# Kernel optimization log

Hardware: AMD Instinct MI355X
Metric: run time of the kernel (lower is better)

## Reference

```python
import jax, jax.numpy as jnp
import numpy as np

DIM = 512
NUM_HEADS = 16
HEAD_DIM = DIM // NUM_HEADS
RES = (32, 32)
SEQ_SCALE = float(np.log(RES[0] * RES[1]))  # seq_length_scale buffer
TABLE = (2 * RES[0] - 1) * (2 * RES[1] - 1)  # 3969
EPS = 1e-12


def setup_inputs() -> dict:
    key = jax.random.key(0)
    ks = jax.random.split(key, 12)
    B, N, C = 8, RES[0] * RES[1], DIM
    s = 0.02
    return {
        "x": jax.random.normal(ks[0], (B, N, C), dtype=jnp.float32),
        "_h": RES[0],
        "_w": RES[1],
        "relative_pos_index": jax.random.randint(ks[1], (N, N), 0, TABLE, dtype=jnp.int32),
        "relative_coords_table": jax.random.uniform(ks[2], (TABLE, 2), dtype=jnp.float32, minval=-1.0, maxval=1.0),
        "qkv_w": jax.random.normal(ks[3], (3 * C, C), dtype=jnp.float32) * s,
        "qkv_b": jnp.zeros((3 * C,), dtype=jnp.float32),
        "proj_w": jax.random.normal(ks[4], (C, C), dtype=jnp.float32) * s,
        "proj_b": jnp.zeros((C,), dtype=jnp.float32),
        "temperature": jnp.full((NUM_HEADS, 1, 1), float(np.log(np.expm1(1.0 / 0.24))), dtype=jnp.float32),
        "query_embedding": jax.random.normal(ks[5], (NUM_HEADS, 1, HEAD_DIM), dtype=jnp.float32) * s,
        "cpb_fc1_w": jax.random.normal(ks[6], (512, 2), dtype=jnp.float32) * s,
        "cpb_fc1_b": jnp.zeros((512,), dtype=jnp.float32),
        "cpb_fc2_w": jax.random.normal(ks[7], (NUM_HEADS, 512), dtype=jnp.float32) * s,
        "cpb_fc2_b": jnp.zeros((NUM_HEADS,), dtype=jnp.float32),
    }


def _l2norm(t):
    # F.normalize(t, dim=-1): x / max(||x||, eps)
    n = jnp.sqrt(jnp.sum(t * t, axis=-1, keepdims=True))
    return t / jnp.maximum(n, EPS)


def reference(x, _h, _w, relative_pos_index, relative_coords_table,
              qkv_w, qkv_b, proj_w, proj_b, temperature, query_embedding,
              cpb_fc1_w, cpb_fc1_b, cpb_fc2_w, cpb_fc2_b):
    B, N, C = x.shape
    H, hd = NUM_HEADS, HEAD_DIM
    # qkv projection -> [B, N, 3H, hd] -> [B, 3H, N, hd]
    qkv = (x @ qkv_w.T + qkv_b).reshape(B, N, 3 * H, hd).transpose(0, 2, 1, 3)
    q, k, v = jnp.split(qkv, 3, axis=1)  # each [B, H, N, hd]
    # CPB MLP relative bias: [T,2] -> [T,H] -> gather -> [H,N,N]
    t = jax.nn.relu(relative_coords_table @ cpb_fc1_w.T + cpb_fc1_b) @ cpb_fc2_w.T + cpb_fc2_b
    rel_bias = t[relative_pos_index].transpose(2, 0, 1)  # [H, N, N]
    # cosine attention with learned softplus temperature and query embedding
    scale = jax.nn.softplus(temperature) * SEQ_SCALE  # [H,1,1]
    qn = (_l2norm(q) + query_embedding[None]) * scale[None]
    kn = _l2norm(k)
    attn = jnp.einsum('bhnd,bhmd->bhnm', qn, kn) + rel_bias[None]
    attn = jax.nn.softmax(attn, axis=-1)
    out = jnp.einsum('bhnm,bhmd->bhnd', attn, v)  # [B,H,N,hd]
    out = out.transpose(0, 2, 1, 3).reshape(B, N, C)
    return out @ proj_w.T + proj_b
```

## Files before the change

kernel.cpp:

```cpp
#include <hip/hip_runtime.h>
#include <cstdint>
#include <cstddef>

typedef _Float16 f16;
typedef _Float16 f16x4 __attribute__((ext_vector_type(4)));
typedef _Float16 f16x8 __attribute__((ext_vector_type(8)));
typedef float f32x4 __attribute__((ext_vector_type(4)));

#define MFMA32(a,b,c) __builtin_amdgcn_mfma_f32_16x16x32_f16((a),(b),(c),0,0,0)
#define MFMA16(a,b,c) __builtin_amdgcn_mfma_f32_16x16x16f16((a),(b),(c),0,0,0)

__device__ __forceinline__ void gload_lds16(const f16* g, f16* l) {
  __builtin_amdgcn_global_load_lds(
      (const __attribute__((address_space(1))) unsigned int*)g,
      (__attribute__((address_space(3))) unsigned int*)l, 16, 0, 0);
}

static constexpr size_t OFF_TCPB = 0;
static constexpr size_t OFF_BIAS = 262144;
static constexpr size_t OFF_XHI  = OFF_BIAS + 33554432;
static constexpr size_t OFF_XLO  = OFF_XHI + 8388608;
static constexpr size_t OFF_WHI  = OFF_XLO + 8388608;
static constexpr size_t OFF_WLO  = OFF_WHI + 1572864;
static constexpr size_t OFF_PW   = OFF_WLO + 1572864;
static constexpr size_t OFF_QHI  = OFF_PW  + 524288;
static constexpr size_t OFF_QLO  = OFF_QHI + 8388608;
static constexpr size_t OFF_KHI  = OFF_QLO + 8388608;
static constexpr size_t OFF_KLO  = OFF_KHI + 8388608;
static constexpr size_t OFF_VT   = OFF_KLO + 8388608;
static constexpr size_t OFF_AO   = OFF_VT  + 8388608;

__global__ __launch_bounds__(256) void k_convert(
    const float* __restrict__ x, const float* __restrict__ qw, const float* __restrict__ pwf,
    f16* __restrict__ xhi, f16* __restrict__ xlo,
    f16* __restrict__ whi, f16* __restrict__ wlo, f16* __restrict__ pw)
{
  int i = blockIdx.x * 256 + threadIdx.x;
  const float4* src; f16* dh; f16* dl; int j;
  if (i < 1048576)      { j = i;           src = (const float4*)x;   dh = xhi; dl = xlo; }
  else if (i < 1245184) { j = i - 1048576; src = (const float4*)qw;  dh = whi; dl = wlo; }
  else                  { j = i - 1245184; src = (const float4*)pwf; dh = pw;  dl = nullptr; }
  float4 v = src[j];
  f16x4 h;
  h[0] = (f16)v.x; h[1] = (f16)v.y; h[2] = (f16)v.z; h[3] = (f16)v.w;
  ((f16x4*)dh)[j] = h;
  if (dl) {
    f16x4 l;
    l[0] = (f16)(v.x - (float)h[0]); l[1] = (f16)(v.y - (float)h[1]);
    l[2] = (f16)(v.z - (float)h[2]); l[3] = (f16)(v.w - (float)h[3]);
    ((f16x4*)dl)[j] = l;
  }
}

__global__ __launch_bounds__(256) void k_cpb(
    const float* __restrict__ table, const float* __restrict__ w1, const float* __restrict__ b1,
    const float* __restrict__ w2, const float* __restrict__ b2, float* __restrict__ t_out)
{
  const int r = blockIdx.x * 4 + (threadIdx.x >> 6);
  const int lane = threadIdx.x & 63;
  if (r >= 3969) return;
  const float c0 = table[2*r], c1 = table[2*r+1];
  const int j0 = lane * 8;
  float h[8];
#pragma unroll
  for (int jj = 0; jj < 8; jj++) {
    int j = j0 + jj;
    float v = c0 * w1[2*j] + c1 * w1[2*j+1] + b1[j];
    h[jj] = v > 0.0f ? v : 0.0f;
  }
  float acc[16];
#pragma unroll
  for (int o = 0; o < 16; o++) {
    const float4* wp = (const float4*)(w2 + o*512 + j0);
    float4 a = wp[0], bb = wp[1];
    acc[o] = a.x*h[0] + a.y*h[1] + a.z*h[2] + a.w*h[3]
           + bb.x*h[4] + bb.y*h[5] + bb.z*h[6] + bb.w*h[7];
  }
#pragma unroll
  for (int o = 0; o < 16; o++) {
    float v = acc[o];
    for (int s = 1; s < 64; s <<= 1) v += __shfl_xor(v, s, 64);
    acc[o] = v;
  }
  if (lane == 0) {
#pragma unroll
    for (int o = 0; o < 16; o++) t_out[r*16 + o] = acc[o] + b2[o];
  }
}

__global__ __launch_bounds__(256) void k_bias(
    const int* __restrict__ idx, const float* __restrict__ t_cpb, f16* __restrict__ bias_t)
{
  const int m4 = blockIdx.x >> 6, ng = blockIdx.x & 63;
  const int h = threadIdx.x >> 4, nl = threadIdx.x & 15;
  const int n = ng*16 + nl;
  int4 I = *(const int4*)(idx + (size_t)n*1024 + m4*4);
  f16x4 o;
  o[0] = (f16)t_cpb[I.x*16 + h];
  o[1] = (f16)t_cpb[I.y*16 + h];
  o[2] = (f16)t_cpb[I.z*16 + h];
  o[3] = (f16)t_cpb[I.w*16 + h];
  *(f16x4*)(bias_t + (((size_t)h*256 + m4)*1024 + n)*4) = o;
}

__global__ __launch_bounds__(256) void k_qkv(
    const f16* __restrict__ xhi, const f16* __restrict__ xlo,
    const f16* __restrict__ whi, const f16* __restrict__ wlo,
    const float* __restrict__ qkvb, const float* __restrict__ temp, const float* __restrict__ qe,
    f16* __restrict__ qh_o, f16* __restrict__ ql_o,
    f16* __restrict__ kh_o, f16* __restrict__ vt_o)
{
  __shared__ __align__(16) f16 Ah[8][64][8];
  __shared__ __align__(16) f16 Al[8][64][8];
  __shared__ __align__(16) f16 Bh[8][64][8];
  __shared__ __align__(16) f16 Bl[8][64][8];
  const int tid = threadIdx.x, lane = tid & 63, w = tid >> 6;
  const int rsel = lane & 15, ksel = lane >> 4;
  const int bx = blockIdx.x & 63, by = blockIdx.x >> 6;
  const int m0 = bx << 7, n0 = by << 7;
  const bool SPLIT = (by < 8);

  const size_t aoff = (size_t)(m0 + w*32 + rsel)*512 + ksel*8;
  const size_t boff = (size_t)(n0 + w*32 + rsel)*512 + ksel*8;
  const f16 *gA0 = xhi + aoff,  *gA1 = gA0 + 16*512;
  const f16 *gAl0 = xlo + aoff, *gAl1 = gAl0 + 16*512;
  const f16 *gB0 = whi + boff,  *gB1 = gB0 + 16*512;
  const f16 *gBl0 = wlo + boff, *gBl1 = gBl0 + 16*512;
  f16 *lA0 = &Ah[2*w][0][0],  *lA1 = &Ah[2*w+1][0][0];
  f16 *lAl0 = &Al[2*w][0][0], *lAl1 = &Al[2*w+1][0][0];
  f16 *lB0 = &Bh[2*w][0][0],  *lB1 = &Bh[2*w+1][0][0];
  f16 *lBl0 = &Bl[2*w][0][0], *lBl1 = &Bl[2*w+1][0][0];

  const f32x4 zero = {0.f, 0.f, 0.f, 0.f};
  f32x4 acc[4][4];
#pragma unroll
  for (int mt = 0; mt < 4; mt++)
#pragma unroll
    for (int nt = 0; nt < 4; nt++) acc[mt][nt] = zero;

  const int mb4 = (w & 1) * 4, nb4 = (w >> 1) * 4;
  for (int k0 = 0; k0 < 512; k0 += 32) {
    __syncthreads();
    gload_lds16(gA0 + k0, lA0);
    gload_lds16(gA1 + k0, lA1);
    gload_lds16(gB0 + k0, lB0);
    gload_lds16(gB1 + k0, lB1);
    if (SPLIT) {
      gload_lds16(gAl0 + k0, lAl0);
      gload_lds16(gAl1 + k0, lAl1);
      gload_lds16(gBl0 + k0, lBl0);
      gload_lds16(gBl1 + k0, lBl1);
    }
    __syncthreads();
    f16x8 bhf[4], blf[4];
#pragma unroll
    for (int nt = 0; nt < 4; nt++) bhf[nt] = ((const f16x8*)&Bh[nb4+nt][0][0])[lane];
    if (SPLIT) {
#pragma unroll
      for (int nt = 0; nt < 4; nt++) blf[nt] = ((const f16x8*)&Bl[nb4+nt][0][0])[lane];
#pragma unroll
      for (int mt = 0; mt < 4; mt++) {
        f16x8 ah = ((const f16x8*)&Ah[mb4+mt][0][0])[lane];
        f16x8 al = ((const f16x8*)&Al[mb4+mt][0][0])[lane];
#pragma unroll
        for (int nt = 0; nt < 4; nt++) {
          acc[mt][nt] = MFMA32(al, bhf[nt], acc[mt][nt]);
          acc[mt][nt] = MFMA32(ah, blf[nt], acc[mt][nt]);
          acc[mt][nt] = MFMA32(ah, bhf[nt], acc[mt][nt]);
        }
      }
    } else {
#pragma unroll
      for (int mt = 0; mt < 4; mt++) {
        f16x8 ah = ((const f16x8*)&Ah[mb4+mt][0][0])[lane];
#pragma unroll
        for (int nt = 0; nt < 4; nt++)
          acc[mt][nt] = MFMA32(ah, bhf[nt], acc[mt][nt]);
      }
    }
  }

  const int mbase = m0 + (w & 1)*64, nbase = n0 + (w >> 1)*64;
  float bc[4];
#pragma unroll
  for (int nt = 0; nt < 4; nt++) bc[nt] = qkvb[nbase + nt*16 + rsel];
#pragma unroll
  for (int mt = 0; mt < 4; mt++)
#pragma unroll
    for (int nt = 0; nt < 4; nt++)
#pragma unroll
      for (int r = 0; r < 4; r++) acc[mt][nt][r] += bc[nt];

  if (by < 8) {
    const bool ISQ = (by < 4);
#pragma unroll
    for (int pair = 0; pair < 2; pair++) {
      const int h = ((nbase - (ISQ ? 0 : 512)) >> 5) + pair;
      float sc = 0.f, qe0 = 0.f, qe1 = 0.f;
      if (ISQ) {
        sc  = log1pf(__expf(temp[h])) * 6.93147180559945f;
        qe0 = qe[h*32 + rsel];
        qe1 = qe[h*32 + 16 + rsel];
      }
      f16* dh = ISQ ? qh_o : kh_o;
#pragma unroll
      for (int mt = 0; mt < 4; mt++) {
        float ss[4];
#pragma unroll
        for (int r = 0; r < 4; r++) {
          float a = acc[mt][2*pair][r], b = acc[mt][2*pair+1][r];
          ss[r] = a*a + b*b;
        }
        for (int s = 1; s < 16; s <<= 1) {
#pragma unroll
          for (int r = 0; r < 4; r++) ss[r] += __shfl_xor(ss[r], s, 64);
        }
#pragma unroll
        for (int r = 0; r < 4; r++) {
          float rn = 1.0f / fmaxf(sqrtf(ss[r]), 1e-12f);
          int m = mbase + mt*16 + ksel*4 + r;
          int b_ = m >> 10, p = m & 1023;
          size_t base = ((size_t)(b_*16 + h)*1024 + p)*32;
          float v0 = acc[mt][2*pair][r] * rn;
          float v1 = acc[mt][2*pair+1][r] * rn;
          if (ISQ) { v0 = (v0 + qe0) * sc; v1 = (v1 + qe1) * sc; }
          f16 h0 = (f16)v0, h1 = (f16)v1;
          dh[base + rsel]      = h0;
          dh[base + 16 + rsel] = h1;
          if (ISQ) {
            ql_o[base + rsel]      = (f16)(v0 - (float)h0);
            ql_o[base + 16 + rsel] = (f16)(v1 - (float)h1);
          }
        }
      }
    }
  } else {
#pragma unroll
    for (int mt = 0; mt < 4; mt++) {
      int m = mbase + mt*16 + ksel*4;
      int b_ = m >> 10, p = m & 1023;
#pragma unroll
      for (int nt = 0; nt < 4; nt++) {
        int n = nbase + nt*16 + rsel;
        int g = (n - 1024) >> 5, d = n & 31;
        f16x4 pk;
#pragma unroll
        for (int r = 0; r < 4; r++) pk[r] = (f16)acc[mt][nt][r];
        *(f16x4*)(vt_o + ((size_t)(b_*16 + g)*32 + d)*1024 + p) = pk;
      }
    }
  }
}

__global__ __launch_bounds__(256, 4) void k_attn(
    const f16* __restrict__ qhi, const f16* __restrict__ qlo,
    const f16* __restrict__ khi, const f16* __restrict__ vt,
    const f16* __restrict__ bias_t,
    f16* __restrict__ po0, f16* __restrict__ po1,
    float2* __restrict__ ml0, float2* __restrict__ ml1)
{
  __shared__ __align__(16) f16 OT[4][32][40];
  const int lane = threadIdx.x & 63, w = threadIdx.x >> 6;
  const int rsel = lane & 15, ksel = lane >> 4;
  const int bid = blockIdx.x;
  const int qt = bid & 7, split = (bid >> 3) & 1, bh = bid >> 4;
  const int h = bh & 15;
  const int q0 = qt*128 + w*32;
  const int mstart = split * 512;

  f16x8 Qh[2], Ql[2];
#pragma unroll
  for (int c = 0; c < 2; c++) {
    size_t o = ((size_t)bh*1024 + q0 + c*16 + rsel)*32 + ksel*8;
    Qh[c] = *(const f16x8*)(qhi + o);
    Ql[c] = *(const f16x8*)(qlo + o);
  }
  const f16* kh_base = khi + (size_t)bh*32768;
  const f16* vt_base = vt  + (size_t)bh*32768;
  const f16* bias_h  = bias_t + (size_t)h*1048576;

  const f32x4 zero = {0.f, 0.f, 0.f, 0.f};
  f32x4 O[2][2];
  float mi[2], li[2];
#pragma unroll
  for (int c = 0; c < 2; c++) {
    O[c][0] = zero; O[c][1] = zero;
    mi[c] = -3.0e38f; li[c] = 0.f;
  }

  f16x8 Kh[2];
  Kh[0] = *(const f16x8*)(kh_base + (size_t)(mstart + rsel)*32 + ksel*8);
  Kh[1] = *(const f16x8*)(kh_base + (size_t)(mstart + 16 + rsel)*32 + ksel*8);

  for (int m0 = mstart; m0 < mstart + 512; m0 += 32) {
    f16x4 Va[2][2], Bb[2][2];
#pragma unroll
    for (int f = 0; f < 2; f++)
#pragma unroll
      for (int dt = 0; dt < 2; dt++)
        Va[f][dt] = *(const f16x4*)(vt_base + (size_t)(dt*16 + rsel)*1024 + m0 + f*16 + ksel*4);
#pragma unroll
    for (int f = 0; f < 2; f++)
#pragma unroll
      for (int c = 0; c < 2; c++)
        Bb[f][c] = *(const f16x4*)(bias_h + (((size_t)(m0 >> 2) + f*4 + ksel)*1024 + q0 + c*16 + rsel)*4);

    f16x8 Kc0 = Kh[0], Kc1 = Kh[1];
    if (m0 < mstart + 480) {
      Kh[0] = *(const f16x8*)(kh_base + (size_t)(m0 + 32 + rsel)*32 + ksel*8);
      Kh[1] = *(const f16x8*)(kh_base + (size_t)(m0 + 48 + rsel)*32 + ksel*8);
    }

    f32x4 St[2][2];
#pragma unroll
    for (int c = 0; c < 2; c++) {
      St[0][c] = MFMA32(Kc0, Ql[c], zero);
      St[0][c] = MFMA32(Kc0, Qh[c], St[0][c]);
      St[1][c] = MFMA32(Kc1, Ql[c], zero);
      St[1][c] = MFMA32(Kc1, Qh[c], St[1][c]);
    }

    f16x4 P16[2][2];
#pragma unroll
    for (int c = 0; c < 2; c++) {
      float s[8];
#pragma unroll
      for (int f = 0; f < 2; f++)
#pragma unroll
        for (int r = 0; r < 4; r++) s[f*4+r] = St[f][c][r] + (float)Bb[f][c][r];
      float cm = s[0];
#pragma unroll
      for (int i = 1; i < 8; i++) cm = fmaxf(cm, s[i]);
      cm = fmaxf(cm, __shfl_xor(cm, 16, 64));
      cm = fmaxf(cm, __shfl_xor(cm, 32, 64));
      float mn = fmaxf(mi[c], cm);
      float alpha = __expf(mi[c] - mn);
      mi[c] = mn;
      float p[8], rs = 0.f;
#pragma unroll
      for (int i = 0; i < 8; i++) { p[i] = __expf(s[i] - mn); rs += p[i]; }
      li[c] = li[c]*alpha + rs;
#pragma unroll
      for (int dt = 0; dt < 2; dt++)
#pragma unroll
        for (int r = 0; r < 4; r++) O[c][dt][r] *= alpha;
#pragma unroll
      for (int f = 0; f < 2; f++)
#pragma unroll
        for (int r = 0; r < 4; r++) P16[f][c][r] = (f16)p[f*4+r];
    }
#pragma unroll
    for (int c = 0; c < 2; c++)
#pragma unroll
      for (int dt = 0; dt < 2; dt++) {
        O[c][dt] = MFMA16(Va[0][dt], P16[0][c], O[c][dt]);
        O[c][dt] = MFMA16(Va[1][dt], P16[1][c], O[c][dt]);
      }
  }

#pragma unroll
  for (int c = 0; c < 2; c++) {
    li[c] += __shfl_xor(li[c], 16, 64);
    li[c] += __shfl_xor(li[c], 32, 64);
    float inv = 1.0f / li[c];
#pragma unroll
    for (int dt = 0; dt < 2; dt++)
#pragma unroll
      for (int r = 0; r < 4; r++)
        OT[w][c*16 + rsel][dt*16 + ksel*4 + r] = (f16)(O[c][dt][r] * inv);
  }
  f16* po_s = split ? po1 : po0;
  float2* ml_s = split ? ml1 : ml0;
  int row = lane >> 1, half = lane & 1;
  f16x8 o0 = *(const f16x8*)(&OT[w][row][half*16]);
  f16x8 o1 = *(const f16x8*)(&OT[w][row][half*16 + 8]);
  f16* outp = po_s + ((size_t)bh*1024 + q0 + row)*32 + half*16;
  *(f16x8*)outp = o0;
  *(f16x8*)(outp + 8) = o1;
  if (lane < 32) {
    int c = lane >> 4;
    float mm = c ? mi[1] : mi[0];
    float ll = c ? li[1] : li[0];
    ml_s[(size_t)bh*1024 + q0 + lane] = make_float2(mm, ll);
  }
}

__global__ __launch_bounds__(256) void k_merge(
    const f16* __restrict__ po0, const f16* __restrict__ po1,
    const float2* __restrict__ ml0, const float2* __restrict__ ml1,
    f16* __restrict__ ao)
{
  int tid = blockIdx.x * 256 + threadIdx.x;
  int h = tid & 15, q = (tid >> 4) & 1023, b = tid >> 14;
  int bh = b*16 + h;
  size_t rec = (size_t)bh*1024 + q;
  float2 a = ml0[rec], c = ml1[rec];
  float M = fmaxf(a.x, c.x);
  float w0 = a.y * __expf(a.x - M);
  float w1 = c.y * __expf(c.x - M);
  float inv = 1.0f / (w0 + w1);
  w0 *= inv; w1 *= inv;
  const f16x8* p0 = (const f16x8*)(po0 + rec*32);
  const f16x8* p1 = (const f16x8*)(po1 + rec*32);
  f16* op = ao + ((size_t)b*1024 + q)*512 + h*32;
#pragma unroll
  for (int i = 0; i < 4; i++) {
    f16x8 x0 = p0[i], x1 = p1[i];
    f16x8 o;
#pragma unroll
    for (int j = 0; j < 8; j++) o[j] = (f16)((float)x0[j]*w0 + (float)x1[j]*w1);
    ((f16x8*)op)[i] = o;
  }
}

__global__ __launch_bounds__(256) void k_proj(
    const f16* __restrict__ A, const f16* __restrict__ Bw,
    const float* __restrict__ pb, float* __restrict__ out)
{
  __shared__ __align__(16) f16 Ah[8][64][8];
  __shared__ __align__(16) f16 Bh[8][64][8];
  const int tid = threadIdx.x, lane = tid & 63, w = tid >> 6;
  const int rsel = lane & 15, ksel = lane >> 4;
  const int bx = blockIdx.x & 63, by = blockIdx.x >> 6;
  const int m0 = bx << 7, n0 = by << 7;
  const f16 *gA0 = A + (size_t)(m0 + w*32 + rsel)*512 + ksel*8,  *gA1 = gA0 + 16*512;
  const f16 *gB0 = Bw + (size_t)(n0 + w*32 + rsel)*512 + ksel*8, *gB1 = gB0 + 16*512;
  f16 *lA0 = &Ah[2*w][0][0], *lA1 = &Ah[2*w+1][0][0];
  f16 *lB0 = &Bh[2*w][0][0], *lB1 = &Bh[2*w+1][0][0];
  const f32x4 zero = {0.f, 0.f, 0.f, 0.f};
  f32x4 acc[4][4];
#pragma unroll
  for (int mt = 0; mt < 4; mt++)
#pragma unroll
    for (int nt = 0; nt < 4; nt++) acc[mt][nt] = zero;
  const int mb4 = (w & 1)*4, nb4 = (w >> 1)*4;
  for (int k0 = 0; k0 < 512; k0 += 32) {
    __syncthreads();
    gload_lds16(gA0 + k0, lA0);
    gload_lds16(gA1 + k0, lA1);
    gload_lds16(gB0 + k0, lB0);
    gload_lds16(gB1 + k0, lB1);
    __syncthreads();
    f16x8 bhf[4];
#pragma unroll
    for (int nt = 0; nt < 4; nt++) bhf[nt] = ((const f16x8*)&Bh[nb4+nt][0][0])[lane];
#pragma unroll
    for (int mt = 0; mt < 4; mt++) {
      f16x8 ah = ((const f16x8*)&Ah[mb4+mt][0][0])[lane];
#pragma unroll
      for (int nt = 0; nt < 4; nt++)
        acc[mt][nt] = MFMA32(ah, bhf[nt], acc[mt][nt]);
    }
  }
  const int mbase = m0 + (w & 1)*64, nbase = n0 + (w >> 1)*64;
  float bc[4];
#pragma unroll
  for (int nt = 0; nt < 4; nt++) bc[nt] = pb[nbase + nt*16 + rsel];
#pragma unroll
  for (int mt = 0; mt < 4; mt++)
#pragma unroll
    for (int nt = 0; nt < 4; nt++)
#pragma unroll
      for (int r = 0; r < 4; r++)
        out[(size_t)(mbase + mt*16 + ksel*4 + r)*512 + nbase + nt*16 + rsel] =
            acc[mt][nt][r] + bc[nt];
}

extern "C" void kernel_launch(void* const* d_in, const int* in_sizes, int n_in,
                              void* d_out, int out_size, void* d_ws, size_t ws_size,
                              hipStream_t stream) {
  const float* x    = (const float*)d_in[0];
  const int*   rpi  = (const int*)d_in[3];
  const float* rct  = (const float*)d_in[4];
  const float* qw   = (const float*)d_in[5];
  const float* qb   = (const float*)d_in[6];
  const float* pwf  = (const float*)d_in[7];
  const float* pbv  = (const float*)d_in[8];
  const float* temp = (const float*)d_in[9];
  const float* qe   = (const float*)d_in[10];
  const float* f1w  = (const float*)d_in[11];
  const float* f1b  = (const float*)d_in[12];
  const float* f2w  = (const float*)d_in[13];
  const float* f2b  = (const float*)d_in[14];

  char* ws = (char*)d_ws;
  float* t_cpb  = (float*)(ws + OFF_TCPB);
  f16* bias_t   = (f16*)(ws + OFF_BIAS);
  f16* xhi = (f16*)(ws + OFF_XHI);
  f16* xlo = (f16*)(ws + OFF_XLO);
  f16* whi = (f16*)(ws + OFF_WHI);
  f16* wlo = (f16*)(ws + OFF_WLO);
  f16* pw  = (f16*)(ws + OFF_PW);
  f16* qhi = (f16*)(ws + OFF_QHI);
  f16* qlo = (f16*)(ws + OFF_QLO);
  f16* khi = (f16*)(ws + OFF_KHI);
  f16* vt  = (f16*)(ws + OFF_VT);
  f16* ao  = (f16*)(ws + OFF_AO);
  f16* po0 = (f16*)(ws + OFF_KLO);
  f16* po1 = (f16*)(ws + OFF_XHI);
  float2* ml0 = (float2*)(ws + OFF_XLO);
  float2* ml1 = ml0 + 131072;

  k_convert<<<5120, 256, 0, stream>>>(x, qw, pwf, xhi, xlo, whi, wlo, pw);
  k_cpb<<<993, 256, 0, stream>>>(rct, f1w, f1b, f2w, f2b, t_cpb);
  k_bias<<<16384, 256, 0, stream>>>(rpi, t_cpb, bias_t);
  k_qkv<<<768, 256, 0, stream>>>(xhi, xlo, whi, wlo, qb, temp, qe,
                                 qhi, qlo, khi, vt);
  k_attn<<<2048, 256, 0, stream>>>(qhi, qlo, khi, vt, bias_t, po0, po1, ml0, ml1);
  k_merge<<<512, 256, 0, stream>>>(po0, po1, ml0, ml1, ao);
  k_proj<<<256, 256, 0, stream>>>(ao, pw, pbv, (float*)d_out);
}
```

Baseline: 310.0 us.

## Drop Q hi/lo split, fold log2e into scales and bias into MFMA accumulator

Q is now stored only as a single fp16 tensor. This removes the low-part buffer, its writes in the QKV kernel and half of the QK^T MFMAs in the attention loop. The softmax moves to exp2: log2(e) is folded into the query scale (ln(1024)*log2e = 10) and into the CPB table, and the merge kernel uses exp2 to match. The relative bias is loaded straight into the MFMA accumulator instead of being added afterwards. The explicit K register prefetch is removed in favour of plain per-iteration loads. The cost is lower precision in the QK^T scores and possibly less latency hiding on the K loads.

Result: no change. 309.9 us (-0.0%).

```diff
diff --git a/kernel.cpp b/kernel.cpp
--- a/kernel.cpp
+++ b/kernel.cpp
@@ -9,6 +9,14 @@
 
 #define MFMA32(a,b,c) __builtin_amdgcn_mfma_f32_16x16x32_f16((a),(b),(c),0,0,0)
 #define MFMA16(a,b,c) __builtin_amdgcn_mfma_f32_16x16x16f16((a),(b),(c),0,0,0)
+
+__device__ __forceinline__ float fexp2(float x) {
+#if __has_builtin(__builtin_amdgcn_exp2f)
+  return __builtin_amdgcn_exp2f(x);
+#else
+  return __expf(x * 0.69314718055994531f);
+#endif
+}
 
 __device__ __forceinline__ void gload_lds16(const f16* g, f16* l) {
   __builtin_amdgcn_global_load_lds(
@@ -84,7 +92,8 @@
   }
   if (lane == 0) {
 #pragma unroll
-    for (int o = 0; o < 16; o++) t_out[r*16 + o] = acc[o] + b2[o];
+    for (int o = 0; o < 16; o++)
+      t_out[r*16 + o] = (acc[o] + b2[o]) * 1.4426950408889634f;
   }
 }
 
@@ -107,8 +116,7 @@
     const f16* __restrict__ xhi, const f16* __restrict__ xlo,
     const f16* __restrict__ whi, const f16* __restrict__ wlo,
     const float* __restrict__ qkvb, const float* __restrict__ temp, const float* __restrict__ qe,
-    f16* __restrict__ qh_o, f16* __restrict__ ql_o,
-    f16* __restrict__ kh_o, f16* __restrict__ vt_o)
+    f16* __restrict__ qh_o, f16* __restrict__ kh_o, f16* __restrict__ vt_o)
 {
   __shared__ __align__(16) f16 Ah[8][64][8];
   __shared__ __align__(16) f16 Al[8][64][8];
@@ -198,7 +206,7 @@
       const int h = ((nbase - (ISQ ? 0 : 512)) >> 5) + pair;
       float sc = 0.f, qe0 = 0.f, qe1 = 0.f;
       if (ISQ) {
-        sc  = log1pf(__expf(temp[h])) * 6.93147180559945f;
+        sc  = log1pf(__expf(temp[h])) * 10.0f;
         qe0 = qe[h*32 + rsel];
         qe1 = qe[h*32 + 16 + rsel];
       }
@@ -224,13 +232,8 @@
           float v0 = acc[mt][2*pair][r] * rn;
           float v1 = acc[mt][2*pair+1][r] * rn;
           if (ISQ) { v0 = (v0 + qe0) * sc; v1 = (v1 + qe1) * sc; }
-          f16 h0 = (f16)v0, h1 = (f16)v1;
-          dh[base + rsel]      = h0;
-          dh[base + 16 + rsel] = h1;
-          if (ISQ) {
-            ql_o[base + rsel]      = (f16)(v0 - (float)h0);
-            ql_o[base + 16 + rsel] = (f16)(v1 - (float)h1);
-          }
+          dh[base + rsel]      = (f16)v0;
+          dh[base + 16 + rsel] = (f16)v1;
         }
       }
     }
@@ -253,8 +256,7 @@
 }
 
 __global__ __launch_bounds__(256, 4) void k_attn(
-    const f16* __restrict__ qhi, const f16* __restrict__ qlo,
-    const f16* __restrict__ khi, const f16* __restrict__ vt,
+    const f16* __restrict__ qhi, const f16* __restrict__ khi, const f16* __restrict__ vt,
     const f16* __restrict__ bias_t,
     f16* __restrict__ po0, f16* __restrict__ po1,
     float2* __restrict__ ml0, float2* __restrict__ ml1)
@@ -268,86 +270,75 @@
   const int q0 = qt*128 + w*32;
   const int mstart = split * 512;
 
-  f16x8 Qh[2], Ql[2];
-#pragma unroll
-  for (int c = 0; c < 2; c++) {
-    size_t o = ((size_t)bh*1024 + q0 + c*16 + rsel)*32 + ksel*8;
-    Qh[c] = *(const f16x8*)(qhi + o);
-    Ql[c] = *(const f16x8*)(qlo + o);
-  }
-  const f16* kh_base = khi + (size_t)bh*32768;
-  const f16* vt_base = vt  + (size_t)bh*32768;
-  const f16* bias_h  = bias_t + (size_t)h*1048576;
-
-  const f32x4 zero = {0.f, 0.f, 0.f, 0.f};
+  f16x8 Qh[2];
+#pragma unroll
+  for (int c = 0; c < 2; c++)
+    Qh[c] = *(const f16x8*)(qhi + ((size_t)bh*1024 + q0 + c*16 + rsel)*32 + ksel*8);
+
+  const f16* kP = khi + (size_t)bh*32768 + (size_t)(mstart + rsel)*32 + ksel*8;
+  const f16* vP = vt  + (size_t)bh*32768 + (size_t)rsel*1024 + mstart + ksel*4;
+  const f16* bP = bias_t + (size_t)h*1048576 +
+                  (((size_t)(mstart >> 2) + ksel)*1024 + q0 + rsel)*4;
+
   f32x4 O[2][2];
   float mi[2], li[2];
 #pragma unroll
   for (int c = 0; c < 2; c++) {
-    O[c][0] = zero; O[c][1] = zero;
+    O[c][0] = (f32x4){0.f,0.f,0.f,0.f};
+    O[c][1] = (f32x4){0.f,0.f,0.f,0.f};
     mi[c] = -3.0e38f; li[c] = 0.f;
   }
 
-  f16x8 Kh[2];
-  Kh[0] = *(const f16x8*)(kh_base + (size_t)(mstart + rsel)*32 + ksel*8);
-  Kh[1] = *(const f16x8*)(kh_base + (size_t)(mstart + 16 + rsel)*32 + ksel*8);
-
-  for (int m0 = mstart; m0 < mstart + 512; m0 += 32) {
-    f16x4 Va[2][2], Bb[2][2];
+  for (int it = 0; it < 16; ++it) {
+    f16x8 K0 = *(const f16x8*)kP;
+    f16x8 K1 = *(const f16x8*)(kP + 512);
+    f16x4 Va[2][2];
+    Va[0][0] = *(const f16x4*)(vP);
+    Va[1][0] = *(const f16x4*)(vP + 16);
+    Va[0][1] = *(const f16x4*)(vP + 16384);
+    Va[1][1] = *(const f16x4*)(vP + 16400);
+    f16x4 Bb[2][2];
+    Bb[0][0] = *(const f16x4*)(bP);
+    Bb[0][1] = *(const f16x4*)(bP + 64);
+    Bb[1][0] = *(const f16x4*)(bP + 16384);
+    Bb[1][1] = *(const f16x4*)(bP + 16448);
+    kP += 1024; vP += 32; bP += 32768;
+
+    f32x4 St[2][2];
 #pragma unroll
     for (int f = 0; f < 2; f++)
 #pragma unroll
-      for (int dt = 0; dt < 2; dt++)
-        Va[f][dt] = *(const f16x4*)(vt_base + (size_t)(dt*16 + rsel)*1024 + m0 + f*16 + ksel*4);
-#pragma unroll
-    for (int f = 0; f < 2; f++)
-#pragma unroll
-      for (int c = 0; c < 2; c++)
-        Bb[f][c] = *(const f16x4*)(bias_h + (((size_t)(m0 >> 2) + f*4 + ksel)*1024 + q0 + c*16 + rsel)*4);
-
-    f16x8 Kc0 = Kh[0], Kc1 = Kh[1];
-    if (m0 < mstart + 480) {
-      Kh[0] = *(const f16x8*)(kh_base + (size_t)(m0 + 32 + rsel)*32 + ksel*8);
-      Kh[1] = *(const f16x8*)(kh_base + (size_t)(m0 + 48 + rsel)*32 + ksel*8);
-    }
-
-    f32x4 St[2][2];
+      for (int c = 0; c < 2; c++) {
+        f32x4 Ci;
+#pragma unroll
+        for (int r = 0; r < 4; r++) Ci[r] = (float)Bb[f][c][r];
+        St[f][c] = MFMA32(f ? K1 : K0, Qh[c], Ci);
+      }
+
+    f16x4 P16[2][2];
 #pragma unroll
     for (int c = 0; c < 2; c++) {
-      St[0][c] = MFMA32(Kc0, Ql[c], zero);
-      St[0][c] = MFMA32(Kc0, Qh[c], St[0][c]);
-      St[1][c] = MFMA32(Kc1, Ql[c], zero);
-      St[1][c] = MFMA32(Kc1, Qh[c], St[1][c]);
-    }
-
-    f16x4 P16[2][2];
-#pragma unroll
-    for (int c = 0; c < 2; c++) {
-      float s[8];
-#pragma unroll
-      for (int f = 0; f < 2; f++)
-#pragma unroll
-        for (int r = 0; r < 4; r++) s[f*4+r] = St[f][c][r] + (float)Bb[f][c][r];
-      float cm = s[0];
-#pragma unroll
-      for (int i = 1; i < 8; i++) cm = fmaxf(cm, s[i]);
+      float cm = fmaxf(fmaxf(fmaxf(St[0][c][0], St[0][c][1]), fmaxf(St[0][c][2], St[0][c][3])),
+                       fmaxf(fmaxf(St[1][c][0], St[1][c][1]), fmaxf(St[1][c][2], St[1][c][3])));
       cm = fmaxf(cm, __shfl_xor(cm, 16, 64));
       cm = fmaxf(cm, __shfl_xor(cm, 32, 64));
       float mn = fmaxf(mi[c], cm);
-      float alpha = __expf(mi[c] - mn);
+      float alpha = fexp2(mi[c] - mn);
       mi[c] = mn;
-      float p[8], rs = 0.f;
-#pragma unroll
-      for (int i = 0; i < 8; i++) { p[i] = __expf(s[i] - mn); rs += p[i]; }
+      float rs = 0.f;
+#pragma unroll
+      for (int f = 0; f < 2; f++)
+#pragma unroll
+        for (int r = 0; r < 4; r++) {
+          float p = fexp2(St[f][c][r] - mn);
+          rs += p;
+          P16[f][c][r] = (f16)p;
+        }
       li[c] = li[c]*alpha + rs;
 #pragma unroll
       for (int dt = 0; dt < 2; dt++)
 #pragma unroll
         for (int r = 0; r < 4; r++) O[c][dt][r] *= alpha;
-#pragma unroll
-      for (int f = 0; f < 2; f++)
-#pragma unroll
-        for (int r = 0; r < 4; r++) P16[f][c][r] = (f16)p[f*4+r];
     }
 #pragma unroll
     for (int c = 0; c < 2; c++)
@@ -396,8 +387,8 @@
   size_t rec = (size_t)bh*1024 + q;
   float2 a = ml0[rec], c = ml1[rec];
   float M = fmaxf(a.x, c.x);
-  float w0 = a.y * __expf(a.x - M);
-  float w1 = c.y * __expf(c.x - M);
+  float w0 = a.y * fexp2(a.x - M);
+  float w1 = c.y * fexp2(c.x - M);
   float inv = 1.0f / (w0 + w1);
   w0 *= inv; w1 *= inv;
   const f16x8* p0 = (const f16x8*)(po0 + rec*32);
@@ -492,7 +483,6 @@
   f16* wlo = (f16*)(ws + OFF_WLO);
   f16* pw  = (f16*)(ws + OFF_PW);
   f16* qhi = (f16*)(ws + OFF_QHI);
-  f16* qlo = (f16*)(ws + OFF_QLO);
   f16* khi = (f16*)(ws + OFF_KHI);
   f16* vt  = (f16*)(ws + OFF_VT);
   f16* ao  = (f16*)(ws + OFF_AO);
@@ -505,8 +495,8 @@
   k_cpb<<<993, 256, 0, stream>>>(rct, f1w, f1b, f2w, f2b, t_cpb);
   k_bias<<<16384, 256, 0, stream>>>(rpi, t_cpb, bias_t);
   k_qkv<<<768, 256, 0, stream>>>(xhi, xlo, whi, wlo, qb, temp, qe,
-                                 qhi, qlo, khi, vt);
-  k_attn<<<2048, 256, 0, stream>>>(qhi, qlo, khi, vt, bias_t, po0, po1, ml0, ml1);
+                                 qhi, khi, vt);
+  k_attn<<<2048, 256, 0, stream>>>(qhi, khi, vt, bias_t, po0, po1, ml0, ml1);
   k_merge<<<512, 256, 0, stream>>>(po0, po1, ml0, ml1, ao);
   k_proj<<<256, 256, 0, stream>>>(ao, pw, pbv, (float*)d_out);
 }
```
